# Kernel tuning notes

Hardware: AMD Instinct MI355X
Metric: run time of the kernel (lower is better)

The kernel has to match this reference:

```python
import jax, jax.numpy as jnp
import numpy as np

B, H, W, D = 64, 56, 56, 128
WS = 7            # window size per axis
NH = 4            # attention heads
L = 2             # transformer layers (layer 1 is shifted)
HID = 4 * D
G1, G2 = H // WS, W // WS
G, N = G1 * G2, WS * WS
SH = WS // 2      # cyclic shift


def _build_attn_mask():
    # faithful port of ShiftWindow mask construction (numpy constants)
    img = np.zeros((H, W), dtype=np.float32)
    sl = (slice(0, -WS), slice(-WS, -SH), slice(-SH, None))
    idx = 0
    for s0 in sl:
        for s1 in sl:
            img[s0, s1] = idx
            idx += 1
    win = img.reshape(G1, WS, G2, WS).transpose(0, 2, 1, 3).reshape(G, N)
    diff = win[:, None, :] - win[:, :, None]          # [G, N, N]
    return jnp.asarray(np.where(diff != 0, -100.0, 0.0).astype(np.float32))

ATTN_MASK = _build_attn_mask()


def setup_inputs() -> dict:
    key = jax.random.key(0)
    ks = jax.random.split(key, 8)
    s = 0.02
    return {
        'x': jax.random.normal(ks[0], (B, H, W, D), jnp.float32),
        'ln1_g': jnp.ones((L, D)), 'ln1_b': jnp.zeros((L, D)),
        'qkv_w': s * jax.random.normal(ks[1], (L, D, 3 * D)), 'qkv_b': jnp.zeros((L, 3 * D)),
        'proj_w': s * jax.random.normal(ks[2], (L, D, D)), 'proj_b': jnp.zeros((L, D)),
        'ln2_g': jnp.ones((L, D)), 'ln2_b': jnp.zeros((L, D)),
        'mlp_w1': s * jax.random.normal(ks[3], (L, D, HID)), 'mlp_b1': jnp.zeros((L, HID)),
        'mlp_w2': s * jax.random.normal(ks[4], (L, HID, D)), 'mlp_b2': jnp.zeros((L, D)),
        'ds_norm_g': jnp.ones((4 * D,)), 'ds_norm_b': jnp.zeros((4 * D,)),
        'ds_w': s * jax.random.normal(ks[5], (4 * D, 2 * D)),
    }


def _ln(x, g, b, eps=1e-5):
    m = jnp.mean(x, -1, keepdims=True)
    v = jnp.mean((x - m) ** 2, -1, keepdims=True)
    return (x - m) * jax.lax.rsqrt(v + eps) * g + b


def _partition(x):
    # [B, H, W, D] -> [B, G, N, D]
    x = x.reshape(B, G1, WS, G2, WS, D).transpose(0, 1, 3, 2, 4, 5)
    return x.reshape(B, G, N, D)


def _unpartition(xw):
    x = xw.reshape(B, G1, G2, WS, WS, D).transpose(0, 1, 3, 2, 4, 5)
    return x.reshape(B, H, W, D)


def _block(xw, mask, i, p):
    # pre-norm window attention
    h = _ln(xw, p['ln1_g'][i], p['ln1_b'][i])
    qkv = h @ p['qkv_w'][i] + p['qkv_b'][i]                 # [B,G,N,3D]
    q, k, v = jnp.split(qkv, 3, axis=-1)
    hd = D // NH
    q = q.reshape(B, G, N, NH, hd)
    k = k.reshape(B, G, N, NH, hd)
    v = v.reshape(B, G, N, NH, hd)
    scores = jnp.einsum('bgnhd,bgmhd->bghnm', q, k) / jnp.sqrt(jnp.float32(hd))
    if mask is not None:
        scores = scores + mask[None, :, None, :, :]         # [1,G,1,N,N]
    attn = jax.nn.softmax(scores, axis=-1)
    o = jnp.einsum('bghnm,bgmhd->bgnhd', attn, v).reshape(B, G, N, D)
    xw = xw + o @ p['proj_w'][i] + p['proj_b'][i]
    # MLP
    h = _ln(xw, p['ln2_g'][i], p['ln2_b'][i])
    h = jax.nn.gelu(h @ p['mlp_w1'][i] + p['mlp_b1'][i])
    return xw + h @ p['mlp_w2'][i] + p['mlp_b2'][i]


def reference(x, ln1_g, ln1_b, qkv_w, qkv_b, proj_w, proj_b, ln2_g, ln2_b,
              mlp_w1, mlp_b1, mlp_w2, mlp_b2, ds_norm_g, ds_norm_b, ds_w):
    p = dict(ln1_g=ln1_g, ln1_b=ln1_b, qkv_w=qkv_w, qkv_b=qkv_b,
             proj_w=proj_w, proj_b=proj_b, ln2_g=ln2_g, ln2_b=ln2_b,
             mlp_w1=mlp_w1, mlp_b1=mlp_b1, mlp_w2=mlp_w2, mlp_b2=mlp_b2)
    xw = _partition(x)
    for i in range(L):
        shift = (i % 2 == 1)
        if shift:
            xw = _partition(jnp.roll(_unpartition(xw), (-SH, -SH), axis=(1, 2)))
            xw = _block(xw, ATTN_MASK, i, p)
            xw = _partition(jnp.roll(_unpartition(xw), (SH, SH), axis=(1, 2)))
        else:
            xw = _block(xw, None, i, p)
    x = _unpartition(xw)
    # Downsample: 2x2 patch merge -> LN -> Linear(4D -> 2D) (no bias)
    x = x.reshape(B, H // 2, 2, W // 2, 2, D).transpose(0, 1, 3, 2, 4, 5)
    x = x.reshape(B, H // 2, W // 2, 4 * D)
    x = _ln(x, ds_norm_g, ds_norm_b) @ ds_w
    return x
```

## Files before the change

### kernel.cpp

```cpp
#include <hip/hip_runtime.h>
#include <hip/hip_bf16.h>


typedef short bf16x8 __attribute__((ext_vector_type(8)));
typedef float f32x4 __attribute__((ext_vector_type(4)));
typedef unsigned short u16;
typedef unsigned int u32;

#define MTOK 200704
#define DSTOK 50176

__device__ __forceinline__ u16 f2b(float f){
  u32 u = __float_as_uint(f);
  u += 0x7fffu + ((u >> 16) & 1u);
  return (u16)(u >> 16);
}
__device__ __forceinline__ float blo(u32 u){ return __uint_as_float(u << 16); }
__device__ __forceinline__ float bhi(u32 u){ return __uint_as_float(u & 0xffff0000u); }

__device__ __forceinline__ float gelu_tanh(float v){
  float u = 0.7978845608028654f * (v + 0.044715f * v * v * v);
  u = fminf(u, 10.f);
  float e = __expf(2.f * u);
  float t = (e - 1.f) / (e + 1.f);
  return 0.5f * v * (1.f + t);
}

__global__ void transpose_cvt(const float* __restrict__ src, u16* __restrict__ dst,
                              int K, int N){
  int e = blockIdx.x * 256 + threadIdx.x;
  if (e >= K * N) return;
  int k = e / N, n = e - k * N;
  dst[n * K + k] = f2b(src[e]);
}

template<int MODE>
__global__ __launch_bounds__(256) void ln_kernel(const float* __restrict__ src,
    const float* __restrict__ gw, const float* __restrict__ bw,
    u16* __restrict__ dst)
{
  int wv = threadIdx.x >> 6, lane = threadIdx.x & 63;
  int t = blockIdx.x * 4 + wv;
  long soff;
  if (MODE == 2) {
    soff = (long)t * 128;
  } else {
    int n = t % 49; int tq = t / 49; int gg = tq & 63; int b_ = tq >> 6;
    int r = n / 7, c = n - 7 * r;
    int h = (gg >> 3) * 7 + r, w = (gg & 7) * 7 + c;
    if (MODE == 1) { h += 3; if (h >= 56) h -= 56; w += 3; if (w >= 56) w -= 56; }
    soff = ((long)((b_ * 56 + h) * 56 + w)) * 128;
  }
  float2 v = *(const float2*)(src + soff + lane * 2);
  float s = v.x + v.y, s2 = v.x * v.x + v.y * v.y;
  #pragma unroll
  for (int o = 32; o; o >>= 1) { s += __shfl_xor(s, o); s2 += __shfl_xor(s2, o); }
  float mean = s * 0.0078125f;
  float var  = s2 * 0.0078125f - mean * mean;
  float rstd = rsqrtf(var + 1e-5f);
  int c0 = lane * 2;
  ushort2 o2;
  o2.x = f2b((v.x - mean) * rstd * gw[c0]   + bw[c0]);
  o2.y = f2b((v.y - mean) * rstd * gw[c0+1] + bw[c0+1]);
  *(ushort2*)(dst + (long)t * 128 + c0) = o2;
}

__global__ __launch_bounds__(256) void ds_ln_kernel(const float* __restrict__ x,
    const float* __restrict__ gw, const float* __restrict__ bw,
    u16* __restrict__ dst)
{
  int wv = threadIdx.x >> 6, lane = threadIdx.x & 63;
  int t = blockIdx.x * 4 + wv;
  int j = t % 28; int tq = t / 28; int i = tq % 28; int b_ = tq / 28;
  int e0 = lane * 8;
  int p = e0 >> 8, q = (e0 >> 7) & 1, d = e0 & 127;
  const float* src = x + ((long)((b_ * 56 + 2*i + p) * 56 + 2*j + q)) * 128 + d;
  float4 a  = *(const float4*)src;
  float4 b4 = *(const float4*)(src + 4);
  float vs[8] = {a.x, a.y, a.z, a.w, b4.x, b4.y, b4.z, b4.w};
  float s = 0.f, s2 = 0.f;
  #pragma unroll
  for (int u = 0; u < 8; u++) { s += vs[u]; s2 += vs[u] * vs[u]; }
  #pragma unroll
  for (int o = 32; o; o >>= 1) { s += __shfl_xor(s, o); s2 += __shfl_xor(s2, o); }
  float mean = s * (1.f / 512.f);
  float var  = s2 * (1.f / 512.f) - mean * mean;
  float rstd = rsqrtf(var + 1e-5f);
  u16 ov[8];
  #pragma unroll
  for (int u = 0; u < 8; u++) ov[u] = f2b((vs[u] - mean) * rstd * gw[e0+u] + bw[e0+u]);
  uint4 o4;
  o4.x = (u32)ov[0] | ((u32)ov[1] << 16);
  o4.y = (u32)ov[2] | ((u32)ov[3] << 16);
  o4.z = (u32)ov[4] | ((u32)ov[5] << 16);
  o4.w = (u32)ov[6] | ((u32)ov[7] << 16);
  *(uint4*)(dst + (long)t * 512 + e0) = o4;
}

template<int MASKED>
__global__ __launch_bounds__(256) void attn_kernel(const u16* __restrict__ qkv,
                                                   u16* __restrict__ obuf)
{
  __shared__ u16 kls[4][49][32];
  __shared__ u16 vls[4][49][32];
  __shared__ float sls[4][49][51];
  int wi = blockIdx.x;
  int g_ = wi & 63;
  long t0 = (long)wi * 49;
  int h = threadIdx.x >> 6, lane = threadIdx.x & 63;
  float qreg[32];
  if (lane < 49) {
    const u16* qp = qkv + (t0 + lane) * 384 + h * 32;
    const u16* kp = qp + 128;
    const u16* vp = qp + 256;
    #pragma unroll
    for (int j = 0; j < 4; j++) {
      *(uint4*)&kls[h][lane][j*8] = *(const uint4*)(kp + j*8);
      *(uint4*)&vls[h][lane][j*8] = *(const uint4*)(vp + j*8);
    }
    #pragma unroll
    for (int j = 0; j < 16; j++) {
      u32 u = *(const u32*)(qp + j*2);
      qreg[2*j]   = blo(u);
      qreg[2*j+1] = bhi(u);
    }
  }
  __syncthreads();
  if (lane >= 49) return;

  int g1b = (g_ >> 3) * 7, g2b = (g_ & 7) * 7;
  int ridn = 0;
  if (MASKED) {
    int rn = lane / 7, cn = lane - 7 * rn;
    int hn = g1b + rn, wn = g2b + cn;
    ridn = (hn < 49 ? 0 : (hn < 53 ? 1 : 2)) * 3 + (wn < 49 ? 0 : (wn < 53 ? 1 : 2));
  }
  float smax = -3.0e38f;
  for (int m = 0; m < 49; m++) {
    const u32* kp32 = (const u32*)&kls[h][m][0];
    float s = 0.f;
    #pragma unroll
    for (int j = 0; j < 16; j++) {
      u32 u = kp32[j];
      s = fmaf(qreg[2*j],   blo(u), s);
      s = fmaf(qreg[2*j+1], bhi(u), s);
    }
    s *= 0.17677669529663687f;
    if (MASKED) {
      int rm = m / 7, cm = m - 7 * rm;
      int hm = g1b + rm, wm = g2b + cm;
      int ridm = (hm < 49 ? 0 : (hm < 53 ? 1 : 2)) * 3 + (wm < 49 ? 0 : (wm < 53 ? 1 : 2));
      if (ridm != ridn) s -= 100.f;
    }
    smax = fmaxf(smax, s);
    sls[h][lane][m] = s;
  }
  float sum = 0.f;
  for (int m = 0; m < 49; m++) {
    float e = __expf(sls[h][lane][m] - smax);
    sum += e;
    sls[h][lane][m] = e;
  }
  float rs = 1.f / sum;
  float o[32];
  #pragma unroll
  for (int d = 0; d < 32; d++) o[d] = 0.f;
  for (int m = 0; m < 49; m++) {
    float p = sls[h][lane][m];
    const u32* vp32 = (const u32*)&vls[h][m][0];
    #pragma unroll
    for (int j = 0; j < 16; j++) {
      u32 u = vp32[j];
      o[2*j]   = fmaf(p, blo(u), o[2*j]);
      o[2*j+1] = fmaf(p, bhi(u), o[2*j+1]);
    }
  }
  u16* op = obuf + (t0 + lane) * 128 + h * 32;
  #pragma unroll
  for (int j = 0; j < 16; j++) {
    ushort2 w2;
    w2.x = f2b(o[2*j]   * rs);
    w2.y = f2b(o[2*j+1] * rs);
    *(ushort2*)(op + 2*j) = w2;
  }
}

template<int K, int EPI>
__global__ __launch_bounds__(256) void gemm_kernel(
    const u16* __restrict__ A, const u16* __restrict__ Bt,
    const float* __restrict__ bias, int Ntot,
    u16* __restrict__ outb, float* __restrict__ outf,
    const float* __restrict__ resbase, int shift)
{
  __shared__ u16 As[128][72];
  __shared__ u16 Bs[128][72];
  const int tid = threadIdx.x;
  const int row0 = blockIdx.x * 128, col0 = blockIdx.y * 128;
  const int wv = tid >> 6, lane = tid & 63;
  const int m_off = (wv >> 1) * 64, n_off = (wv & 1) * 64;
  const int lr = lane & 15, lk = (lane >> 4) * 8;

  f32x4 acc[4][4];
  const f32x4 zero4 = {0.f, 0.f, 0.f, 0.f};
  #pragma unroll
  for (int a1 = 0; a1 < 4; a1++)
    #pragma unroll
    for (int a2 = 0; a2 < 4; a2++) acc[a1][a2] = zero4;

  for (int k0 = 0; k0 < K; k0 += 64) {
    __syncthreads();
    #pragma unroll
    for (int j = 0; j < 4; j++) {
      int ch = tid + 256 * j;
      int r = ch >> 3, cc = ch & 7;
      *(uint4*)(&As[r][cc*8]) = *(const uint4*)(A  + (long)(row0 + r) * K + k0 + cc*8);
      *(uint4*)(&Bs[r][cc*8]) = *(const uint4*)(Bt + (long)(col0 + r) * K + k0 + cc*8);
    }
    __syncthreads();
    #pragma unroll
    for (int kk = 0; kk < 64; kk += 32) {
      bf16x8 af[4], bfr[4];
      #pragma unroll
      for (int mi = 0; mi < 4; mi++)
        af[mi] = *(const bf16x8*)(&As[m_off + mi*16 + lr][kk + lk]);
      #pragma unroll
      for (int ni = 0; ni < 4; ni++)
        bfr[ni] = *(const bf16x8*)(&Bs[n_off + ni*16 + lr][kk + lk]);
      #pragma unroll
      for (int mi = 0; mi < 4; mi++)
        #pragma unroll
        for (int ni = 0; ni < 4; ni++)
          acc[mi][ni] = __builtin_amdgcn_mfma_f32_16x16x32_bf16(
              af[mi], bfr[ni], acc[mi][ni], 0, 0, 0);
    }
  }

  #pragma unroll
  for (int mi = 0; mi < 4; mi++) {
    #pragma unroll
    for (int j = 0; j < 4; j++) {
      int grow = row0 + m_off + mi*16 + (lane >> 4) * 4 + j;
      long obase = 0;
      if (EPI == 2) {
        int n = grow % 49; int tq = grow / 49; int gg = tq & 63; int b_ = tq >> 6;
        int r = n / 7, c = n - 7 * r;
        int hh = (gg >> 3) * 7 + r, ww = (gg & 7) * 7 + c;
        if (shift) { hh += 3; if (hh >= 56) hh -= 56; ww += 3; if (ww >= 56) ww -= 56; }
        obase = ((long)((b_ * 56 + hh) * 56 + ww)) * 128;
      }
      #pragma unroll
      for (int ni = 0; ni < 4; ni++) {
        int gcol = col0 + n_off + ni*16 + lr;
        float v = acc[mi][ni][j];
        if (EPI == 0) {
          v += bias[gcol];
          outb[(long)grow * Ntot + gcol] = f2b(v);
        } else if (EPI == 1) {
          v = gelu_tanh(v + bias[gcol]);
          outb[(long)grow * Ntot + gcol] = f2b(v);
        } else if (EPI == 2) {
          v += bias[gcol];
          outf[obase + gcol] = resbase[obase + gcol] + v;
        } else if (EPI == 3) {
          v += bias[gcol];
          outf[(long)grow * 128 + gcol] += v;
        } else {
          outf[(long)grow * Ntot + gcol] = v;
        }
      }
    }
  }
}

extern "C" void kernel_launch(void* const* d_in, const int* in_sizes, int n_in,
                              void* d_out, int out_size, void* d_ws, size_t ws_size,
                              hipStream_t stream)
{
  const float* x_in   = (const float*)d_in[0];
  const float* ln1_g  = (const float*)d_in[1];
  const float* ln1_b  = (const float*)d_in[2];
  const float* qkv_w  = (const float*)d_in[3];
  const float* qkv_b  = (const float*)d_in[4];
  const float* proj_w = (const float*)d_in[5];
  const float* proj_b = (const float*)d_in[6];
  const float* ln2_g  = (const float*)d_in[7];
  const float* ln2_b  = (const float*)d_in[8];
  const float* w1     = (const float*)d_in[9];
  const float* b1     = (const float*)d_in[10];
  const float* w2     = (const float*)d_in[11];
  const float* b2     = (const float*)d_in[12];
  const float* dsg    = (const float*)d_in[13];
  const float* dsb    = (const float*)d_in[14];
  const float* dsw    = (const float*)d_in[15];

  float* x_ws   = (float*)d_ws;
  u16* buf_h    = (u16*)(x_ws + (long)MTOK * 128);
  u16* buf_o    = buf_h;
  u16* buf_big  = buf_h + (long)MTOK * 128;
  u16* wts      = buf_big + (long)MTOK * 512;
  u16* qkv_wt   = wts;
  u16* proj_wt  = qkv_wt  + 2 * 49152;
  u16* w1t      = proj_wt + 2 * 16384;
  u16* w2t      = w1t     + 2 * 65536;
  u16* ds_wt    = w2t     + 2 * 65536;

  for (int i = 0; i < 2; i++) {
    transpose_cvt<<<(49152+255)/256, 256, 0, stream>>>(qkv_w  + i*49152, qkv_wt  + i*49152, 128, 384);
    transpose_cvt<<<(16384+255)/256, 256, 0, stream>>>(proj_w + i*16384, proj_wt + i*16384, 128, 128);
    transpose_cvt<<<(65536+255)/256, 256, 0, stream>>>(w1     + i*65536, w1t     + i*65536, 128, 512);
    transpose_cvt<<<(65536+255)/256, 256, 0, stream>>>(w2     + i*65536, w2t     + i*65536, 512, 128);
  }
  transpose_cvt<<<(131072+255)/256, 256, 0, stream>>>(dsw, ds_wt, 512, 256);

  for (int i = 0; i < 2; i++) {
    if (i == 0) ln_kernel<0><<<MTOK/4, 256, 0, stream>>>(x_in, ln1_g,       ln1_b,       buf_h);
    else        ln_kernel<1><<<MTOK/4, 256, 0, stream>>>(x_ws, ln1_g + 128, ln1_b + 128, buf_h);
    gemm_kernel<128,0><<<dim3(MTOK/128, 3), 256, 0, stream>>>(
        buf_h, qkv_wt + i*49152, qkv_b + i*384, 384, buf_big, nullptr, nullptr, 0);
    if (i == 0) attn_kernel<0><<<4096, 256, 0, stream>>>(buf_big, buf_o);
    else        attn_kernel<1><<<4096, 256, 0, stream>>>(buf_big, buf_o);
    gemm_kernel<128,2><<<dim3(MTOK/128, 1), 256, 0, stream>>>(
        buf_o, proj_wt + i*16384, proj_b + i*128, 128, nullptr, x_ws,
        (i == 0 ? x_in : (const float*)x_ws), i);
    ln_kernel<2><<<MTOK/4, 256, 0, stream>>>(x_ws, ln2_g + i*128, ln2_b + i*128, buf_h);
    gemm_kernel<128,1><<<dim3(MTOK/128, 4), 256, 0, stream>>>(
        buf_h, w1t + i*65536, b1 + i*512, 512, buf_big, nullptr, nullptr, 0);
    gemm_kernel<512,3><<<dim3(MTOK/128, 1), 256, 0, stream>>>(
        buf_big, w2t + i*65536, b2 + i*128, 128, nullptr, x_ws, x_ws, 0);
  }

  ds_ln_kernel<<<DSTOK/4, 256, 0, stream>>>(x_ws, dsg, dsb, buf_h);
  gemm_kernel<512,4><<<dim3(DSTOK/128, 2), 256, 0, stream>>>(
      buf_h, ds_wt, nullptr, 256, nullptr, (float*)d_out, nullptr, 0);
}
```

Measured before the change: 1.362 ms.

## Rewrite window attention to use bf16 MFMA for QK^T and PV

Replaces the scalar per-lane window attention kernel with one that computes QK^T and P·V using 16x16x32 bf16 MFMA instructions. The 49-token window is padded to 64 with clamped rows and masked columns, and the softmax is done on accumulator fragments with cross-lane shuffles. Probabilities are staged through LDS as bf16 for the second MFMA. The goal is to remove the heavy scalar FMA and LDS traffic of the old kernel. The cost is padding waste, bf16 rounding of probabilities, and strided scalar gathers for V.

```diff
diff --git a/kernel.cpp b/kernel.cpp
--- a/kernel.cpp
+++ b/kernel.cpp
@@ -98,91 +98,125 @@
 }
 
 template<int MASKED>
-__global__ __launch_bounds__(256) void attn_kernel(const u16* __restrict__ qkv,
-                                                   u16* __restrict__ obuf)
-{
-  __shared__ u16 kls[4][49][32];
-  __shared__ u16 vls[4][49][32];
-  __shared__ float sls[4][49][51];
-  int wi = blockIdx.x;
-  int g_ = wi & 63;
-  long t0 = (long)wi * 49;
-  int h = threadIdx.x >> 6, lane = threadIdx.x & 63;
-  float qreg[32];
-  if (lane < 49) {
-    const u16* qp = qkv + (t0 + lane) * 384 + h * 32;
-    const u16* kp = qp + 128;
-    const u16* vp = qp + 256;
+__global__ __launch_bounds__(256) void attn_mfma(const u16* __restrict__ qkv,
+                                                 u16* __restrict__ obuf)
+{
+  __shared__ u16 Pls_all[4][64][72];
+  const int h = threadIdx.x >> 6;
+  const int lane = threadIdx.x & 63;
+  const int c = lane & 15, g = lane >> 4;
+  const int wi = blockIdx.x;
+  const int g_ = wi & 63;
+  const long t0 = (long)wi * 49;
+  u16 (*Pls)[72] = Pls_all[h];
+
+  bf16x8 qf[4], kf[4];
+  #pragma unroll
+  for (int mi = 0; mi < 4; mi++) {
+    int r = 16*mi + c; r = r > 48 ? 48 : r;
+    qf[mi] = *(const bf16x8*)(qkv + (t0 + r)*384 + h*32 + g*8);
+  }
+  #pragma unroll
+  for (int ni = 0; ni < 4; ni++) {
+    int r = 16*ni + c; r = r > 48 ? 48 : r;
+    kf[ni] = *(const bf16x8*)(qkv + (t0 + r)*384 + 128 + h*32 + g*8);
+  }
+
+  f32x4 acc[4][4];
+  const f32x4 zero4 = {0.f, 0.f, 0.f, 0.f};
+  #pragma unroll
+  for (int mi = 0; mi < 4; mi++)
+    #pragma unroll
+    for (int ni = 0; ni < 4; ni++)
+      acc[mi][ni] = __builtin_amdgcn_mfma_f32_16x16x32_bf16(qf[mi], kf[ni], zero4, 0, 0, 0);
+
+  bf16x8 vf[2][2];
+  #pragma unroll
+  for (int ni2 = 0; ni2 < 2; ni2++)
+    #pragma unroll
+    for (int ks = 0; ks < 2; ks++)
+      #pragma unroll
+      for (int jj = 0; jj < 8; jj++) {
+        int k = ks*32 + 8*g + jj; k = k > 48 ? 48 : k;
+        vf[ni2][ks][jj] = (short)qkv[(t0 + k)*384 + 256 + h*32 + 16*ni2 + c];
+      }
+
+  int rid_c[4];
+  int g1b = 0, g2b = 0;
+  if (MASKED) {
+    g1b = (g_ >> 3) * 7; g2b = (g_ & 7) * 7;
+    #pragma unroll
+    for (int ni = 0; ni < 4; ni++) {
+      int col = 16*ni + c; col = col > 48 ? 48 : col;
+      int cr = col / 7, cc = col - 7*cr;
+      int hh = g1b + cr, ww = g2b + cc;
+      rid_c[ni] = (hh < 49 ? 0 : (hh < 53 ? 1 : 2)) * 3 + (ww < 49 ? 0 : (ww < 53 ? 1 : 2));
+    }
+  }
+
+  #pragma unroll
+  for (int mi = 0; mi < 4; mi++) {
     #pragma unroll
     for (int j = 0; j < 4; j++) {
-      *(uint4*)&kls[h][lane][j*8] = *(const uint4*)(kp + j*8);
-      *(uint4*)&vls[h][lane][j*8] = *(const uint4*)(vp + j*8);
-    }
-    #pragma unroll
-    for (int j = 0; j < 16; j++) {
-      u32 u = *(const u32*)(qp + j*2);
-      qreg[2*j]   = blo(u);
-      qreg[2*j+1] = bhi(u);
-    }
-  }
+      int rr = 16*mi + 4*g + j;
+      int rid_r = 0;
+      if (MASKED) {
+        int r2 = rr > 48 ? 48 : rr;
+        int rh = r2 / 7, rw = r2 - 7*rh;
+        int hh = g1b + rh, ww = g2b + rw;
+        rid_r = (hh < 49 ? 0 : (hh < 53 ? 1 : 2)) * 3 + (ww < 49 ? 0 : (ww < 53 ? 1 : 2));
+      }
+      float sv[4];
+      #pragma unroll
+      for (int ni = 0; ni < 4; ni++) {
+        float s = acc[mi][ni][j] * 0.17677669529663687f;
+        int col = 16*ni + c;
+        if (col >= 49) s = -1e30f;
+        else if (MASKED && rid_c[ni] != rid_r) s -= 100.f;
+        sv[ni] = s;
+      }
+      float m4 = fmaxf(fmaxf(sv[0], sv[1]), fmaxf(sv[2], sv[3]));
+      #pragma unroll
+      for (int o = 1; o <= 8; o <<= 1) m4 = fmaxf(m4, __shfl_xor(m4, o));
+      float p[4], sum = 0.f;
+      #pragma unroll
+      for (int ni = 0; ni < 4; ni++) { p[ni] = __expf(sv[ni] - m4); sum += p[ni]; }
+      #pragma unroll
+      for (int o = 1; o <= 8; o <<= 1) sum += __shfl_xor(sum, o);
+      float rs = 1.f / sum;
+      #pragma unroll
+      for (int ni = 0; ni < 4; ni++)
+        Pls[rr][16*ni + c] = f2b(p[ni] * rs);
+    }
+  }
+
   __syncthreads();
-  if (lane >= 49) return;
-
-  int g1b = (g_ >> 3) * 7, g2b = (g_ & 7) * 7;
-  int ridn = 0;
-  if (MASKED) {
-    int rn = lane / 7, cn = lane - 7 * rn;
-    int hn = g1b + rn, wn = g2b + cn;
-    ridn = (hn < 49 ? 0 : (hn < 53 ? 1 : 2)) * 3 + (wn < 49 ? 0 : (wn < 53 ? 1 : 2));
-  }
-  float smax = -3.0e38f;
-  for (int m = 0; m < 49; m++) {
-    const u32* kp32 = (const u32*)&kls[h][m][0];
-    float s = 0.f;
-    #pragma unroll
-    for (int j = 0; j < 16; j++) {
-      u32 u = kp32[j];
-      s = fmaf(qreg[2*j],   blo(u), s);
-      s = fmaf(qreg[2*j+1], bhi(u), s);
-    }
-    s *= 0.17677669529663687f;
-    if (MASKED) {
-      int rm = m / 7, cm = m - 7 * rm;
-      int hm = g1b + rm, wm = g2b + cm;
-      int ridm = (hm < 49 ? 0 : (hm < 53 ? 1 : 2)) * 3 + (wm < 49 ? 0 : (wm < 53 ? 1 : 2));
-      if (ridm != ridn) s -= 100.f;
-    }
-    smax = fmaxf(smax, s);
-    sls[h][lane][m] = s;
-  }
-  float sum = 0.f;
-  for (int m = 0; m < 49; m++) {
-    float e = __expf(sls[h][lane][m] - smax);
-    sum += e;
-    sls[h][lane][m] = e;
-  }
-  float rs = 1.f / sum;
-  float o[32];
-  #pragma unroll
-  for (int d = 0; d < 32; d++) o[d] = 0.f;
-  for (int m = 0; m < 49; m++) {
-    float p = sls[h][lane][m];
-    const u32* vp32 = (const u32*)&vls[h][m][0];
-    #pragma unroll
-    for (int j = 0; j < 16; j++) {
-      u32 u = vp32[j];
-      o[2*j]   = fmaf(p, blo(u), o[2*j]);
-      o[2*j+1] = fmaf(p, bhi(u), o[2*j+1]);
-    }
-  }
-  u16* op = obuf + (t0 + lane) * 128 + h * 32;
-  #pragma unroll
-  for (int j = 0; j < 16; j++) {
-    ushort2 w2;
-    w2.x = f2b(o[2*j]   * rs);
-    w2.y = f2b(o[2*j+1] * rs);
-    *(ushort2*)(op + 2*j) = w2;
-  }
+
+  f32x4 accO[4][2];
+  #pragma unroll
+  for (int mi = 0; mi < 4; mi++)
+    #pragma unroll
+    for (int ni2 = 0; ni2 < 2; ni2++) accO[mi][ni2] = zero4;
+  #pragma unroll
+  for (int mi = 0; mi < 4; mi++)
+    #pragma unroll
+    for (int ks = 0; ks < 2; ks++) {
+      bf16x8 pa = *(const bf16x8*)(&Pls[16*mi + c][ks*32 + g*8]);
+      #pragma unroll
+      for (int ni2 = 0; ni2 < 2; ni2++)
+        accO[mi][ni2] = __builtin_amdgcn_mfma_f32_16x16x32_bf16(pa, vf[ni2][ks], accO[mi][ni2], 0, 0, 0);
+    }
+
+  #pragma unroll
+  for (int mi = 0; mi < 4; mi++)
+    #pragma unroll
+    for (int ni2 = 0; ni2 < 2; ni2++)
+      #pragma unroll
+      for (int j = 0; j < 4; j++) {
+        int r = 16*mi + 4*g + j;
+        if (r < 49)
+          obuf[(t0 + r)*128 + h*32 + 16*ni2 + c] = f2b(accO[mi][ni2][j]);
+      }
 }
 
 template<int K, int EPI>
@@ -317,8 +351,8 @@
     else        ln_kernel<1><<<MTOK/4, 256, 0, stream>>>(x_ws, ln1_g + 128, ln1_b + 128, buf_h);
     gemm_kernel<128,0><<<dim3(MTOK/128, 3), 256, 0, stream>>>(
         buf_h, qkv_wt + i*49152, qkv_b + i*384, 384, buf_big, nullptr, nullptr, 0);
-    if (i == 0) attn_kernel<0><<<4096, 256, 0, stream>>>(buf_big, buf_o);
-    else        attn_kernel<1><<<4096, 256, 0, stream>>>(buf_big, buf_o);
+    if (i == 0) attn_mfma<0><<<4096, 256, 0, stream>>>(buf_big, buf_o);
+    else        attn_mfma<1><<<4096, 256, 0, stream>>>(buf_big, buf_o);
     gemm_kernel<128,2><<<dim3(MTOK/128, 1), 256, 0, stream>>>(
         buf_o, proj_wt + i*16384, proj_b + i*128, 128, nullptr, x_ws,
         (i == 0 ? x_in : (const float*)x_ws), i);
```

After: 1.111 ms. 18.4% less time.
